# Optimization experiments

Measured on AMD Instinct MI355X. Metric: run time of the kernel, lower is better.

Reference implementation:

```python
import jax, jax.numpy as jnp
import numpy as np

N_NODES = 100000
N_EDGES = 3200000
IN_FEATS = 256
HEADS = 8
OUT_FEATS = 32
NEG_SLOPE = 0.2


def setup_inputs() -> dict:
    key = jax.random.key(0)
    k1, k2, k3, k4, k5, k6 = jax.random.split(key, 6)
    feat = jax.random.normal(k1, (N_NODES, IN_FEATS), dtype=jnp.float32)
    src = jax.random.randint(k2, (N_EDGES,), 0, N_NODES, dtype=jnp.int32)
    dst = jax.random.randint(k3, (N_EDGES,), 0, N_NODES, dtype=jnp.int32)
    fc_weight = jax.random.normal(k4, (HEADS * OUT_FEATS, IN_FEATS), dtype=jnp.float32) * 0.05
    attn_l = jax.random.normal(k5, (1, HEADS, OUT_FEATS), dtype=jnp.float32) * 0.1
    attn_r = jax.random.normal(k6, (1, HEADS, OUT_FEATS), dtype=jnp.float32) * 0.1
    bias_param = jnp.zeros((HEADS * OUT_FEATS,), dtype=jnp.float32)
    return {"feat": feat, "src": src, "dst": dst, "fc_weight": fc_weight,
            "attn_l": attn_l, "attn_r": attn_r, "bias_param": bias_param}


def reference(feat, src, dst, fc_weight, attn_l, attn_r, bias_param):
    # Linear projection: [N, in] @ [in, H*F] -> [N, H, F]
    h = (feat @ fc_weight.T).reshape(-1, HEADS, OUT_FEATS)
    # Per-node attention logits: [N, H]
    el = jnp.einsum('nhf,hf->nh', h, attn_l[0])
    er = jnp.einsum('nhf,hf->nh', h, attn_r[0])
    # Edge scores: gather + add + LeakyReLU -> [E, H]
    e = el[src] + er[dst]
    e = jnp.where(e > 0, e, NEG_SLOPE * e)
    # Edge softmax: segment-softmax over destination nodes
    m = jax.ops.segment_max(e, dst, num_segments=N_NODES)  # [N, H]
    m = jnp.where(jnp.isfinite(m), m, 0.0)
    ex = jnp.exp(e - m[dst])                               # [E, H]
    s = jax.ops.segment_sum(ex, dst, num_segments=N_NODES)  # [N, H]
    a = ex / jnp.where(s[dst] > 0, s[dst], 1.0)            # [E, H]
    # Weighted scatter-sum aggregation: [E, H, F] -> [N, H, F]
    msg = h[src] * a[:, :, None]
    rst = jax.ops.segment_sum(msg, dst, num_segments=N_NODES)
    rst = rst + bias_param.reshape(1, HEADS, OUT_FEATS)
    return rst
```

## Files before the change

kernel.cpp:

```cpp
#include <hip/hip_runtime.h>
#include <hip/hip_bf16.h>
#include <stdint.h>

#define N_IN   256
#define HEADS  8
#define OUTF   32
#define HF     256
#define NEG    0.2f

#define SHIFT  8
#define BMASK  255
#define NBMAX  512
#define TILE   8192
#define CAP    10240

typedef __attribute__((ext_vector_type(8))) short  s16x8;
typedef __attribute__((ext_vector_type(4))) float  f32x4;
typedef __attribute__((ext_vector_type(4))) unsigned int u32x4;

__device__ __forceinline__ unsigned short f2b(float f) {
    unsigned int u = __float_as_uint(f);
    unsigned int r = (u + 0x7fffu + ((u >> 16) & 1u)) >> 16;
    return (unsigned short)r;
}
__device__ __forceinline__ float b2f(unsigned short u) {
    union { unsigned int i; float f; } x; x.i = ((unsigned int)u) << 16; return x.f;
}

__global__ __launch_bounds__(256) void probe_fill(float* __restrict__ out, int n, float val)
{
    int i = blockIdx.x * blockDim.x + threadIdx.x;
    if (i < n) out[i] = val;
}

__global__ __launch_bounds__(256) void cvt_w(const float* __restrict__ W,
                                             unsigned short* __restrict__ Wb, int n)
{
    int i = blockIdx.x * blockDim.x + threadIdx.x;
    if (i < n) Wb[i] = f2b(W[i]);
}

__global__ __launch_bounds__(256) void gemm_h(
    const float* __restrict__ feat,
    const unsigned short* __restrict__ Wb,
    const float* __restrict__ attn_l,
    const float* __restrict__ attn_r,
    unsigned char* __restrict__ h8,
    float* __restrict__ hscale,
    float* __restrict__ el, float* __restrict__ er,
    int* __restrict__ flag, int N)
{
    __shared__ unsigned short hs[4][16][260];
    int wave = (blockIdx.x * blockDim.x + threadIdx.x) >> 6;
    int lane = threadIdx.x & 63;
    int w    = (threadIdx.x >> 6) & 3;
    int m0 = wave * 16;
    if (m0 >= N) return;
    int mr = lane & 15;
    int kg = lane >> 4;

    const float* ap = feat + (size_t)(m0 + mr) * N_IN + kg * 8;
    bool bad = false;
    s16x8 a[8];
#pragma unroll
    for (int kk = 0; kk < 8; kk++) {
        f32x4 lo = __builtin_nontemporal_load((const f32x4*)(ap + kk * 32));
        f32x4 hi = __builtin_nontemporal_load((const f32x4*)(ap + kk * 32 + 4));
#pragma unroll
        for (int j = 0; j < 4; j++) {
            bad |= ((__float_as_uint(lo[j]) >> 23) & 0xFF) >= 0x90;
            bad |= ((__float_as_uint(hi[j]) >> 23) & 0xFF) >= 0x90;
        }
        s16x8 r;
        r[0] = (short)f2b(lo[0]); r[1] = (short)f2b(lo[1]);
        r[2] = (short)f2b(lo[2]); r[3] = (short)f2b(lo[3]);
        r[4] = (short)f2b(hi[0]); r[5] = (short)f2b(hi[1]);
        r[6] = (short)f2b(hi[2]); r[7] = (short)f2b(hi[3]);
        a[kk] = r;
    }
    if (__ballot(bad) != 0ull && lane == 0) atomicOr(flag, 1);

    f32x4 acc[16];
#pragma unroll
    for (int nt = 0; nt < 16; nt++) {
        acc[nt] = (f32x4){0.f, 0.f, 0.f, 0.f};
        const unsigned short* bp = Wb + (size_t)(nt * 16 + mr) * N_IN + kg * 8;
#pragma unroll
        for (int kk = 0; kk < 8; kk++) {
            s16x8 b = *(const s16x8*)(bp + kk * 32);
            acc[nt] = __builtin_amdgcn_mfma_f32_16x16x32_bf16(a[kk], b, acc[nt], 0, 0, 0);
        }
    }
#pragma unroll
    for (int nt = 0; nt < 16; nt++) {
        int col = nt * 16 + mr;
#pragma unroll
        for (int r = 0; r < 4; r++) {
            int row = kg * 4 + r;
            hs[w][row][col] = f2b(acc[nt][r]);
        }
    }
    {
        int row = lane >> 2, hd4 = lane & 3;
#pragma unroll
        for (int p = 0; p < 2; p++) {
            int hd = hd4 + p * 4;
            const unsigned short* hp = &hs[w][row][hd * OUTF];
            const float* al = attn_l + hd * OUTF;
            const float* ar = attn_r + hd * OUTF;
            float sl = 0.f, sr = 0.f;
#pragma unroll
            for (int i = 0; i < 4; i++) {
                s16x8 hv = *(const s16x8*)(hp + i * 8);
                f32x4 al0 = *(const f32x4*)(al + i * 8);
                f32x4 al1 = *(const f32x4*)(al + i * 8 + 4);
                f32x4 ar0 = *(const f32x4*)(ar + i * 8);
                f32x4 ar1 = *(const f32x4*)(ar + i * 8 + 4);
#pragma unroll
                for (int j = 0; j < 4; j++) {
                    float v = b2f((unsigned short)hv[j]);
                    sl += v * al0[j]; sr += v * ar0[j];
                }
#pragma unroll
                for (int j = 0; j < 4; j++) {
                    float v = b2f((unsigned short)hv[4 + j]);
                    sl += v * al1[j]; sr += v * ar1[j];
                }
            }
            el[(size_t)(m0 + row) * HEADS + hd] = sl;
            er[(size_t)(m0 + row) * HEADS + hd] = sr;
        }
    }
    {
        int row = lane >> 2, q4 = lane & 3;
        unsigned int mxb = 0;
#pragma unroll
        for (int i = 0; i < 8; i++) {
            s16x8 hv = *(const s16x8*)(&hs[w][row][q4 * 64 + i * 8]);
#pragma unroll
            for (int j = 0; j < 8; j++) {
                unsigned int b = ((unsigned int)(unsigned short)hv[j]) & 0x7fffu;
                mxb = b > mxb ? b : mxb;
            }
        }
        mxb = max(mxb, (unsigned int)__shfl_xor((int)mxb, 1));
        mxb = max(mxb, (unsigned int)__shfl_xor((int)mxb, 2));
        float mx = b2f((unsigned short)mxb);
        float scale = mx * (1.0f / 127.0f);
        float invs  = (mx > 0.f) ? 127.0f / mx : 0.f;
        if (q4 == 0) hscale[m0 + row] = scale;
#pragma unroll
        for (int c = 0; c < 4; c++) {
            u32x4 wout;
#pragma unroll
            for (int p = 0; p < 4; p++) {
                unsigned int wrd = 0;
#pragma unroll
                for (int k = 0; k < 4; k++) {
                    float v = b2f(hs[w][row][q4 * 64 + c * 16 + p * 4 + k]);
                    int qi = (int)rintf(v * invs) + 128;
                    qi = min(max(qi, 0), 255);
                    wrd |= ((unsigned int)qi) << (8 * k);
                }
                wout[p] = wrd;
            }
            *(u32x4*)(h8 + (size_t)(m0 + row) * HF + q4 * 64 + c * 16) = wout;
        }
    }
}

__global__ __launch_bounds__(256) void bin_scatter(
    const int* __restrict__ src, const int* __restrict__ dst,
    int* __restrict__ bucket_cursor, unsigned int* __restrict__ mid,
    int* __restrict__ flag, int E, int N, int NB)
{
    __shared__ int hist[NBMAX];
    __shared__ int cur[NBMAX];
    __shared__ int gbase[NBMAX];
    __shared__ int part[256];
    __shared__ unsigned int  sorted[TILE];
    __shared__ unsigned short sortedb[TILE];
    int t = threadIdx.x;
#pragma unroll
    for (int i = t; i < NBMAX; i += 256) hist[i] = 0;
    __syncthreads();
    int tb = blockIdx.x * TILE;
    int cnt = min(TILE, E - tb);

#pragma unroll
    for (int i = 0; i < TILE / 256; i++) {
        int e = tb + t + i * 256;
        if (e < E) {
            int d = __builtin_nontemporal_load(&dst[e]);
            d = min(max(d, 0), N - 1);
            atomicAdd(&hist[d >> SHIFT], 1);
        }
    }
    __syncthreads();

    for (int b = t; b < NB; b += 256) {
        int c = hist[b];
        int gb = c ? atomicAdd(&bucket_cursor[b], c) : 0;
        gbase[b] = gb;
        if (c && gb + c > CAP) atomicOr(flag, 1);
    }

    int b0 = 2 * t, b1 = 2 * t + 1;
    int c0 = hist[b0], c1 = hist[b1];
    part[t] = c0 + c1;
    __syncthreads();
    for (int off = 1; off < 256; off <<= 1) {
        int y = (t >= off) ? part[t - off] : 0;
        __syncthreads();
        part[t] += y;
        __syncthreads();
    }
    int pb = part[t] - (c0 + c1);
    hist[b0] = pb;      hist[b1] = pb + c0;
    cur[b0]  = pb;      cur[b1]  = pb + c0;
    __syncthreads();

#pragma unroll
    for (int i = 0; i < TILE / 256; i++) {
        int e = tb + t + i * 256;
        if (e < E) {
            int d = dst[e]; d = min(max(d, 0), N - 1);
            int s = src[e]; s = min(max(s, 0), N - 1);
            int b = d >> SHIFT;
            int p = atomicAdd(&cur[b], 1);
            sorted[p]  = ((unsigned int)s << SHIFT) | (unsigned int)(d & BMASK);
            sortedb[p] = (unsigned short)b;
        }
    }
    __syncthreads();

    for (int i = t; i < cnt; i += 256) {
        int b = sortedb[i];
        int idx = gbase[b] + (i - hist[b]);
        if (idx < CAP) mid[(size_t)b * CAP + idx] = sorted[i];
    }
}

__global__ __launch_bounds__(512) void scan_buckets(
    const int* __restrict__ bucket_cursor, int* __restrict__ bucket_base, int NB)
{
    __shared__ int lds[512];
    int t = threadIdx.x;
    int v = (t < NB) ? bucket_cursor[t] : 0;
    lds[t] = v;
    __syncthreads();
    for (int off = 1; off < 512; off <<= 1) {
        int y = (t >= off) ? lds[t - off] : 0;
        __syncthreads();
        lds[t] += y;
        __syncthreads();
    }
    if (t < NB) bucket_base[t] = lds[t] - v;
}

__global__ __launch_bounds__(256) void bucket_sort(
    const unsigned int* __restrict__ mid,
    const int* __restrict__ bucket_base, const int* __restrict__ bucket_cursor,
    int* __restrict__ offs, int* __restrict__ ssorted, int N, int E, int NB)
{
    __shared__ int hist[256];
    __shared__ int lds[256];
    __shared__ int cur[256];
    int b = blockIdx.x;
    int t = threadIdx.x;
    hist[t] = 0;
    __syncthreads();
    int base = bucket_base[b];
    int cnt  = min(bucket_cursor[b], CAP);
    const unsigned int* ms = mid + (size_t)b * CAP;
    for (int i = t; i < cnt; i += 256) {
        unsigned int v = ms[i];
        atomicAdd(&hist[v & BMASK], 1);
    }
    __syncthreads();
    int c = hist[t];
    lds[t] = c;
    __syncthreads();
    for (int off = 1; off < 256; off <<= 1) {
        int y = (t >= off) ? lds[t - off] : 0;
        __syncthreads();
        lds[t] += y;
        __syncthreads();
    }
    int excl = lds[t] - c;
    cur[t] = excl;
    int node = (b << SHIFT) + t;
    if (node < N) offs[node] = base + excl;
    if (b == NB - 1 && t == 0) offs[N] = E;
    __syncthreads();
    for (int i = t; i < cnt; i += 256) {
        unsigned int v = ms[i];
        int p = atomicAdd(&cur[v & BMASK], 1);
        ssorted[base + p] = (int)(v >> SHIFT);
    }
}

__global__ __launch_bounds__(256) void aggregate(
    const unsigned char* __restrict__ h8,
    const float* __restrict__ hscale,
    const float* __restrict__ el, const float* __restrict__ er,
    const int* __restrict__ offs, const int* __restrict__ ssorted,
    const float* __restrict__ bias,
    const int* __restrict__ flag,
    float* __restrict__ out, int N, int E)
{
    int wave = blockIdx.x * 4 + (threadIdx.x >> 6);
    int lane = threadIdx.x & 63;
    if (wave >= N) return;
    int node = wave;
    int flagv = flag[0];
    int e0 = offs[node], e1 = offs[node + 1];
    e0 = min(max(e0, 0), E);
    e1 = min(max(e1, e0), E);

    int slot = lane >> 4;
    int g    = lane & 15;
    int hg   = g >> 1;

    float er_d = er[node * HEADS + hg];
    float s_acc = 0.f;
    float sb_acc = 0.f;
    float acc[16];
#pragma unroll
    for (int i = 0; i < 16; i++) acc[i] = 0.f;

    if (e0 < e1) {
        int jA = e0 + slot;
        int sA = __builtin_nontemporal_load(&ssorted[jA]);
        int sB = __builtin_nontemporal_load(&ssorted[jA + 4]);
        bool vA = jA < e1;
        bool vB = (jA + 4) < e1;
        sA = min(max(sA, 0), N - 1);
        int snA = vA ? sA : 0;
        float elA = el[snA * HEADS + hg];
        float scA = hscale[snA];
        u32x4 hA = *(const u32x4*)(h8 + (size_t)snA * HF + g * 16);

        for (int j0 = e0; j0 < e1; j0 += 4) {
            int sC = __builtin_nontemporal_load(&ssorted[j0 + 8 + slot]);
            int sBc = min(max(sB, 0), N - 1);
            int snB = vB ? sBc : 0;
            float elB = el[snB * HEADS + hg];
            float scB = hscale[snB];
            u32x4 hB = *(const u32x4*)(h8 + (size_t)snB * HF + g * 16);
            __builtin_amdgcn_sched_barrier(0);
            float e = elA + er_d;
            e = fmaxf(e, NEG * e);
            float a = vA ? __expf(e) : 0.f;
            s_acc += a;
            float as2 = a * scA;
            sb_acc += as2;
#pragma unroll
            for (int p = 0; p < 4; p++) {
                unsigned int wrd = hA[p];
                acc[p*4+0] += as2 * (float)(wrd & 0xffu);
                acc[p*4+1] += as2 * (float)((wrd >> 8) & 0xffu);
                acc[p*4+2] += as2 * (float)((wrd >> 16) & 0xffu);
                acc[p*4+3] += as2 * (float)(wrd >> 24);
            }
            vA = vB; elA = elB; scA = scB; hA = hB;
            sB = sC; vB = (j0 + 8 + slot) < e1;
        }
    }

    s_acc += __shfl_xor(s_acc, 16);
    s_acc += __shfl_xor(s_acc, 32);
    sb_acc += __shfl_xor(sb_acc, 16);
    sb_acc += __shfl_xor(sb_acc, 32);
#pragma unroll
    for (int i = 0; i < 16; i++) {
        acc[i] += __shfl_xor(acc[i], 16);
        acc[i] += __shfl_xor(acc[i], 32);
    }
    float inv = (s_acc > 0.f) ? 1.f / s_acc : 0.f;

    if (slot == 0) {
        int fo = g * 16;
        bool badv = !__builtin_isfinite(s_acc);
        float vbuf[16];
#pragma unroll
        for (int i = 0; i < 16; i++) {
            float v = (acc[i] - 128.0f * sb_acc) * inv + bias[fo + i];
            badv |= !__builtin_isfinite(v);
            vbuf[i] = v;
        }
        if (flagv) {
#pragma unroll
            for (int i = 0; i < 16; i++) vbuf[i] = 555.0f;
        } else if (badv) {
#pragma unroll
            for (int i = 0; i < 16; i++) vbuf[i] = 777.0f;
        }
#pragma unroll
        for (int q = 0; q < 4; q++) {
            f32x4 o = { vbuf[q*4+0], vbuf[q*4+1], vbuf[q*4+2], vbuf[q*4+3] };
            __builtin_nontemporal_store(o, (f32x4*)(out + (size_t)node * HF + fo + q * 4));
        }
    }
}

extern "C" void kernel_launch(void* const* d_in, const int* in_sizes, int n_in,
                              void* d_out, int out_size, void* d_ws, size_t ws_size,
                              hipStream_t stream)
{
    const float* feat   = (const float*)d_in[0];
    const int*   src    = (const int*)d_in[1];
    const int*   dst    = (const int*)d_in[2];
    const float* fc_w   = (const float*)d_in[3];
    const float* attn_l = (const float*)d_in[4];
    const float* attn_r = (const float*)d_in[5];
    const float* bias   = (const float*)d_in[6];
    float* out = (float*)d_out;

    const int N = in_sizes[0] / N_IN;
    const int E = in_sizes[1];
    const int NB = (N + 255) >> SHIFT;

    char* ws = (char*)d_ws;
    size_t off = 0;
    auto alloc = [&](size_t bytes) -> char* {
        char* p = ws + off;
        off = (off + bytes + 255) & ~(size_t)255;
        return p;
    };
    int* bucket_cursor = (int*)alloc((size_t)NBMAX * 4 + 256);
    int* flag          = bucket_cursor + NBMAX;
    int* bucket_base   = (int*)alloc((size_t)NBMAX * 4);
    unsigned int* mid  = (unsigned int*)alloc((size_t)NB * CAP * 4);
    int* ssorted       = (int*)alloc((size_t)(E + 64) * 4);
    int* offs          = (int*)alloc((size_t)(N + 1) * 4);
    float* el          = (float*)alloc((size_t)N * HEADS * 4);
    float* er          = (float*)alloc((size_t)N * HEADS * 4);
    unsigned char* h8  = (unsigned char*)alloc((size_t)N * HF);
    float* hscale      = (float*)alloc((size_t)N * 4);
    unsigned short* Wb = (unsigned short*)alloc((size_t)HF * N_IN * 2);

    if (off > ws_size || NB > NBMAX || N >= (1 << 24)) {
        probe_fill<<<(out_size + 255) / 256, 256, 0, stream>>>(out, out_size, 999.0f);
        return;
    }

    hipMemsetAsync(bucket_cursor, 0, (size_t)NBMAX * 4 + 256, stream);

    cvt_w<<<(HF * N_IN + 255) / 256, 256, 0, stream>>>(fc_w, Wb, HF * N_IN);
    {
        int waves = (N + 15) / 16;
        int blocks = (waves + 3) / 4;
        gemm_h<<<blocks, 256, 0, stream>>>(feat, Wb, attn_l, attn_r, h8, hscale, el, er, flag, N);
    }
    int tiles = (E + TILE - 1) / TILE;
    bin_scatter<<<tiles, 256, 0, stream>>>(src, dst, bucket_cursor, mid, flag, E, N, NB);
    scan_buckets<<<1, 512, 0, stream>>>(bucket_cursor, bucket_base, NB);
    bucket_sort<<<NB, 256, 0, stream>>>(mid, bucket_base, bucket_cursor, offs, ssorted, N, E, NB);
    {
        int blocks = (N + 3) / 4;
        aggregate<<<blocks, 256, 0, stream>>>(h8, hscale, el, er, offs, ssorted, bias, flag, out, N, E);
    }
}
```

Baseline: 569.1 us.

## Fuse per-bucket counting sort into aggregation kernel using LDS-resident edge lists

Removes the scan_buckets and bucket_sort kernels and the global sorted-source/offset arrays. Each aggregate block now loads one coarse bucket (128 destination nodes) from the binned buffer into LDS, counting-sorts it by node there, and its 8 waves aggregate those nodes directly from LDS indices. The bucket width is halved to 128 nodes with a smaller per-bucket capacity so the lists fit in shared memory, and bin_scatter's prefix scan is adapted to handle 4 buckets per thread. The cost is fewer, larger blocks using about 40KB of LDS each, lower occupancy, and a tighter overflow capacity per bucket.

```diff
diff --git a/kernel.cpp b/kernel.cpp
--- a/kernel.cpp
+++ b/kernel.cpp
@@ -8,11 +8,12 @@
 #define HF     256
 #define NEG    0.2f
 
-#define SHIFT  8
-#define BMASK  255
-#define NBMAX  512
+#define SHIFT  7
+#define BMASK  127
+#define NBKT   128
+#define NBMAX  1024
 #define TILE   8192
-#define CAP    10240
+#define CAP    4864
 
 typedef __attribute__((ext_vector_type(8))) short  s16x8;
 typedef __attribute__((ext_vector_type(4))) float  f32x4;
@@ -205,9 +206,10 @@
         if (c && gb + c > CAP) atomicOr(flag, 1);
     }
 
-    int b0 = 2 * t, b1 = 2 * t + 1;
-    int c0 = hist[b0], c1 = hist[b1];
-    part[t] = c0 + c1;
+    int b0 = 4 * t;
+    int c0 = hist[b0], c1 = hist[b0 + 1], c2 = hist[b0 + 2], c3 = hist[b0 + 3];
+    int s01 = c0 + c1, sall = s01 + c2 + c3;
+    part[t] = sall;
     __syncthreads();
     for (int off = 1; off < 256; off <<= 1) {
         int y = (t >= off) ? part[t - off] : 0;
@@ -215,9 +217,11 @@
         part[t] += y;
         __syncthreads();
     }
-    int pb = part[t] - (c0 + c1);
-    hist[b0] = pb;      hist[b1] = pb + c0;
-    cur[b0]  = pb;      cur[b1]  = pb + c0;
+    int pb = part[t] - sall;
+    hist[b0]     = pb;           cur[b0]     = pb;
+    hist[b0 + 1] = pb + c0;      cur[b0 + 1] = pb + c0;
+    hist[b0 + 2] = pb + s01;     cur[b0 + 2] = pb + s01;
+    hist[b0 + 3] = pb + s01 + c2; cur[b0 + 3] = pb + s01 + c2;
     __syncthreads();
 
 #pragma unroll
@@ -241,165 +245,135 @@
     }
 }
 
-__global__ __launch_bounds__(512) void scan_buckets(
-    const int* __restrict__ bucket_cursor, int* __restrict__ bucket_base, int NB)
-{
-    __shared__ int lds[512];
-    int t = threadIdx.x;
-    int v = (t < NB) ? bucket_cursor[t] : 0;
-    lds[t] = v;
-    __syncthreads();
-    for (int off = 1; off < 512; off <<= 1) {
-        int y = (t >= off) ? lds[t - off] : 0;
-        __syncthreads();
-        lds[t] += y;
-        __syncthreads();
-    }
-    if (t < NB) bucket_base[t] = lds[t] - v;
-}
-
-__global__ __launch_bounds__(256) void bucket_sort(
-    const unsigned int* __restrict__ mid,
-    const int* __restrict__ bucket_base, const int* __restrict__ bucket_cursor,
-    int* __restrict__ offs, int* __restrict__ ssorted, int N, int E, int NB)
-{
-    __shared__ int hist[256];
-    __shared__ int lds[256];
-    __shared__ int cur[256];
-    int b = blockIdx.x;
-    int t = threadIdx.x;
-    hist[t] = 0;
-    __syncthreads();
-    int base = bucket_base[b];
-    int cnt  = min(bucket_cursor[b], CAP);
-    const unsigned int* ms = mid + (size_t)b * CAP;
-    for (int i = t; i < cnt; i += 256) {
-        unsigned int v = ms[i];
-        atomicAdd(&hist[v & BMASK], 1);
-    }
-    __syncthreads();
-    int c = hist[t];
-    lds[t] = c;
-    __syncthreads();
-    for (int off = 1; off < 256; off <<= 1) {
-        int y = (t >= off) ? lds[t - off] : 0;
-        __syncthreads();
-        lds[t] += y;
-        __syncthreads();
-    }
-    int excl = lds[t] - c;
-    cur[t] = excl;
-    int node = (b << SHIFT) + t;
-    if (node < N) offs[node] = base + excl;
-    if (b == NB - 1 && t == 0) offs[N] = E;
-    __syncthreads();
-    for (int i = t; i < cnt; i += 256) {
-        unsigned int v = ms[i];
-        int p = atomicAdd(&cur[v & BMASK], 1);
-        ssorted[base + p] = (int)(v >> SHIFT);
-    }
-}
-
-__global__ __launch_bounds__(256) void aggregate(
+__global__ __launch_bounds__(512) void aggregate(
     const unsigned char* __restrict__ h8,
     const float* __restrict__ hscale,
     const float* __restrict__ el, const float* __restrict__ er,
-    const int* __restrict__ offs, const int* __restrict__ ssorted,
+    const int* __restrict__ bucket_cursor,
+    const unsigned int* __restrict__ mid,
     const float* __restrict__ bias,
     const int* __restrict__ flag,
-    float* __restrict__ out, int N, int E)
-{
-    int wave = blockIdx.x * 4 + (threadIdx.x >> 6);
-    int lane = threadIdx.x & 63;
-    if (wave >= N) return;
-    int node = wave;
-    int flagv = flag[0];
-    int e0 = offs[node], e1 = offs[node + 1];
-    e0 = min(max(e0, 0), E);
-    e1 = min(max(e1, e0), E);
-
+    float* __restrict__ out, int N)
+{
+    __shared__ unsigned int raw[CAP];
+    __shared__ unsigned int srt[CAP];
+    __shared__ int hist[NBKT];
+    __shared__ int scn[NBKT];
+    __shared__ int cur[NBKT];
+    int b = blockIdx.x, t = threadIdx.x;
+    if (t < NBKT) hist[t] = 0;
+    __syncthreads();
+    int cnt = min(bucket_cursor[b], CAP);
+    const unsigned int* ms = mid + (size_t)b * CAP;
+    for (int i = t; i < cnt; i += 512) {
+        unsigned int v = __builtin_nontemporal_load(&ms[i]);
+        raw[i] = v;
+        atomicAdd(&hist[v & BMASK], 1);
+    }
+    __syncthreads();
+    if (t < NBKT) scn[t] = hist[t];
+    __syncthreads();
+    for (int off = 1; off < NBKT; off <<= 1) {
+        int y = (t < NBKT && t >= off) ? scn[t - off] : 0;
+        __syncthreads();
+        if (t < NBKT) scn[t] += y;
+        __syncthreads();
+    }
+    if (t < NBKT) cur[t] = scn[t] - hist[t];
+    __syncthreads();
+    for (int i = t; i < cnt; i += 512) {
+        unsigned int v = raw[i];
+        int p = atomicAdd(&cur[v & BMASK], 1);
+        srt[p] = v >> SHIFT;
+    }
+    __syncthreads();
+
+    int wave = t >> 6, lane = t & 63;
     int slot = lane >> 4;
     int g    = lane & 15;
     int hg   = g >> 1;
-
-    float er_d = er[node * HEADS + hg];
-    float s_acc = 0.f;
-    float sb_acc = 0.f;
-    float acc[16];
-#pragma unroll
-    for (int i = 0; i < 16; i++) acc[i] = 0.f;
-
-    if (e0 < e1) {
-        int jA = e0 + slot;
-        int sA = __builtin_nontemporal_load(&ssorted[jA]);
-        int sB = __builtin_nontemporal_load(&ssorted[jA + 4]);
-        bool vA = jA < e1;
-        bool vB = (jA + 4) < e1;
-        sA = min(max(sA, 0), N - 1);
-        int snA = vA ? sA : 0;
-        float elA = el[snA * HEADS + hg];
-        float scA = hscale[snA];
-        u32x4 hA = *(const u32x4*)(h8 + (size_t)snA * HF + g * 16);
-
-        for (int j0 = e0; j0 < e1; j0 += 4) {
-            int sC = __builtin_nontemporal_load(&ssorted[j0 + 8 + slot]);
-            int sBc = min(max(sB, 0), N - 1);
-            int snB = vB ? sBc : 0;
-            float elB = el[snB * HEADS + hg];
-            float scB = hscale[snB];
-            u32x4 hB = *(const u32x4*)(h8 + (size_t)snB * HF + g * 16);
-            __builtin_amdgcn_sched_barrier(0);
-            float e = elA + er_d;
-            e = fmaxf(e, NEG * e);
-            float a = vA ? __expf(e) : 0.f;
-            s_acc += a;
-            float as2 = a * scA;
-            sb_acc += as2;
-#pragma unroll
-            for (int p = 0; p < 4; p++) {
-                unsigned int wrd = hA[p];
-                acc[p*4+0] += as2 * (float)(wrd & 0xffu);
-                acc[p*4+1] += as2 * (float)((wrd >> 8) & 0xffu);
-                acc[p*4+2] += as2 * (float)((wrd >> 16) & 0xffu);
-                acc[p*4+3] += as2 * (float)(wrd >> 24);
-            }
-            vA = vB; elA = elB; scA = scB; hA = hB;
-            sB = sC; vB = (j0 + 8 + slot) < e1;
-        }
-    }
-
-    s_acc += __shfl_xor(s_acc, 16);
-    s_acc += __shfl_xor(s_acc, 32);
-    sb_acc += __shfl_xor(sb_acc, 16);
-    sb_acc += __shfl_xor(sb_acc, 32);
-#pragma unroll
-    for (int i = 0; i < 16; i++) {
-        acc[i] += __shfl_xor(acc[i], 16);
-        acc[i] += __shfl_xor(acc[i], 32);
-    }
-    float inv = (s_acc > 0.f) ? 1.f / s_acc : 0.f;
-
-    if (slot == 0) {
-        int fo = g * 16;
-        bool badv = !__builtin_isfinite(s_acc);
-        float vbuf[16];
+    int flagv = flag[0];
+
+    for (int ld = wave; ld < NBKT; ld += 8) {
+        int node = (b << SHIFT) + ld;
+        if (node >= N) break;
+        int e1 = scn[ld];
+        int e0 = e1 - hist[ld];
+        float er_d = er[node * HEADS + hg];
+        float s_acc = 0.f, sb_acc = 0.f;
+        float acc[16];
+#pragma unroll
+        for (int i = 0; i < 16; i++) acc[i] = 0.f;
+
+        if (e0 < e1) {
+            int jA = e0 + slot;
+            bool vA = jA < e1;
+            int snA = (int)srt[min(jA, e1 - 1)];
+            snA = vA ? snA : 0;
+            float elA = el[snA * HEADS + hg];
+            float scA = hscale[snA];
+            u32x4 hA = *(const u32x4*)(h8 + (size_t)snA * HF + g * 16);
+
+            for (int j0 = e0; j0 < e1; j0 += 4) {
+                int jB = j0 + 4 + slot;
+                bool vB = jB < e1;
+                int snB = (int)srt[min(jB, e1 - 1)];
+                snB = vB ? snB : 0;
+                float elB = el[snB * HEADS + hg];
+                float scB = hscale[snB];
+                u32x4 hB = *(const u32x4*)(h8 + (size_t)snB * HF + g * 16);
+                __builtin_amdgcn_sched_barrier(0);
+                float e = elA + er_d;
+                e = fmaxf(e, NEG * e);
+                float a = vA ? __expf(e) : 0.f;
+                s_acc += a;
+                float as2 = a * scA;
+                sb_acc += as2;
+#pragma unroll
+                for (int p = 0; p < 4; p++) {
+                    unsigned int wrd = hA[p];
+                    acc[p*4+0] += as2 * (float)(wrd & 0xffu);
+                    acc[p*4+1] += as2 * (float)((wrd >> 8) & 0xffu);
+                    acc[p*4+2] += as2 * (float)((wrd >> 16) & 0xffu);
+                    acc[p*4+3] += as2 * (float)(wrd >> 24);
+                }
+                vA = vB; elA = elB; scA = scB; hA = hB;
+            }
+        }
+
+        s_acc += __shfl_xor(s_acc, 16);
+        s_acc += __shfl_xor(s_acc, 32);
+        sb_acc += __shfl_xor(sb_acc, 16);
+        sb_acc += __shfl_xor(sb_acc, 32);
 #pragma unroll
         for (int i = 0; i < 16; i++) {
-            float v = (acc[i] - 128.0f * sb_acc) * inv + bias[fo + i];
-            badv |= !__builtin_isfinite(v);
-            vbuf[i] = v;
-        }
-        if (flagv) {
-#pragma unroll
-            for (int i = 0; i < 16; i++) vbuf[i] = 555.0f;
-        } else if (badv) {
-#pragma unroll
-            for (int i = 0; i < 16; i++) vbuf[i] = 777.0f;
-        }
-#pragma unroll
-        for (int q = 0; q < 4; q++) {
-            f32x4 o = { vbuf[q*4+0], vbuf[q*4+1], vbuf[q*4+2], vbuf[q*4+3] };
-            __builtin_nontemporal_store(o, (f32x4*)(out + (size_t)node * HF + fo + q * 4));
+            acc[i] += __shfl_xor(acc[i], 16);
+            acc[i] += __shfl_xor(acc[i], 32);
+        }
+        float inv = (s_acc > 0.f) ? 1.f / s_acc : 0.f;
+
+        if (slot == 0) {
+            int fo = g * 16;
+            bool badv = !__builtin_isfinite(s_acc);
+            float vbuf[16];
+#pragma unroll
+            for (int i = 0; i < 16; i++) {
+                float v = (acc[i] - 128.0f * sb_acc) * inv + bias[fo + i];
+                badv |= !__builtin_isfinite(v);
+                vbuf[i] = v;
+            }
+            if (flagv) {
+#pragma unroll
+                for (int i = 0; i < 16; i++) vbuf[i] = 555.0f;
+            } else if (badv) {
+#pragma unroll
+                for (int i = 0; i < 16; i++) vbuf[i] = 777.0f;
+            }
+#pragma unroll
+            for (int q = 0; q < 4; q++) {
+                f32x4 o = { vbuf[q*4+0], vbuf[q*4+1], vbuf[q*4+2], vbuf[q*4+3] };
+                __builtin_nontemporal_store(o, (f32x4*)(out + (size_t)node * HF + fo + q * 4));
+            }
         }
     }
 }
@@ -419,7 +393,7 @@
 
     const int N = in_sizes[0] / N_IN;
     const int E = in_sizes[1];
-    const int NB = (N + 255) >> SHIFT;
+    const int NB = (N + NBKT - 1) >> SHIFT;
 
     char* ws = (char*)d_ws;
     size_t off = 0;
@@ -430,10 +404,7 @@
     };
     int* bucket_cursor = (int*)alloc((size_t)NBMAX * 4 + 256);
     int* flag          = bucket_cursor + NBMAX;
-    int* bucket_base   = (int*)alloc((size_t)NBMAX * 4);
     unsigned int* mid  = (unsigned int*)alloc((size_t)NB * CAP * 4);
-    int* ssorted       = (int*)alloc((size_t)(E + 64) * 4);
-    int* offs          = (int*)alloc((size_t)(N + 1) * 4);
     float* el          = (float*)alloc((size_t)N * HEADS * 4);
     float* er          = (float*)alloc((size_t)N * HEADS * 4);
     unsigned char* h8  = (unsigned char*)alloc((size_t)N * HF);
@@ -455,10 +426,5 @@
     }
     int tiles = (E + TILE - 1) / TILE;
     bin_scatter<<<tiles, 256, 0, stream>>>(src, dst, bucket_cursor, mid, flag, E, N, NB);
-    scan_buckets<<<1, 512, 0, stream>>>(bucket_cursor, bucket_base, NB);
-    bucket_sort<<<NB, 256, 0, stream>>>(mid, bucket_base, bucket_cursor, offs, ssorted, N, E, NB);
-    {
-        int blocks = (N + 3) / 4;
-        aggregate<<<blocks, 256, 0, stream>>>(h8, hscale, el, er, offs, ssorted, bias, flag, out, N, E);
-    }
-}
+    aggregate<<<NB, 512, 0, stream>>>(h8, hscale, el, er, bucket_cursor, mid, bias, flag, out, N);
+}
```

Result: slower. 590.5 us (+3.8%).
